# Optimization experiments

Measured on AMD Instinct MI355X. Metric: run time of the kernel, lower is better.

Reference implementation:

```python
import jax, jax.numpy as jnp
import numpy as np

RADIUS = 1.0  # df.ball_point(1, ...) -> radius 1, nsample 1


def ball_point(src_xyz, query_xyz, radius=RADIUS):
    """Ball query with nsample=1.
    src_xyz [B,M,3], query_xyz [B,N,3] -> idx [B,N] (first src point within
    radius, 0 if none), mask [B,N] (True if any src point within radius)."""
    d2 = jnp.sum((query_xyz[:, :, None, :] - src_xyz[:, None, :, :]) ** 2, axis=-1)  # [B,N,M]
    within = d2 < radius * radius
    idx = jnp.argmax(within, axis=-1)          # first True along M, else 0
    mask = jnp.any(within, axis=-1)
    return idx, mask


def gather_group(points, idx):
    """index_points_group with K=1: points [B,M,C], idx [B,N] -> [B,N,1,C]."""
    g = jnp.take_along_axis(points, idx[:, :, None], axis=1)  # [B,N,C]
    return g[:, :, None, :]


def _layer_loss(att_xyz, bat_xyz, att_feat, bat_feat):
    # feats come in as [B,C,N]; original does .permute(0,2,1)
    att_feat = jnp.transpose(att_feat, (0, 2, 1))  # [B,N_att,C]
    bat_feat = jnp.transpose(bat_feat, (0, 2, 1))  # [B,N_bat,C]
    bat_idx, _ = ball_point(bat_xyz, bat_xyz)
    att_idx, mask = ball_point(att_xyz, bat_xyz)
    group_att = jnp.concatenate(
        [gather_group(att_xyz, att_idx), gather_group(att_feat, att_idx)], axis=-1)  # [B,N,1,3+C]
    group_bat = jnp.concatenate(
        [gather_group(bat_xyz, bat_idx), gather_group(bat_feat, bat_idx)], axis=-1)
    m = mask[:, :, None, None].astype(group_att.dtype)  # broadcast over K=1 and C
    group_att = group_att * m
    group_bat = group_bat * m
    return jnp.mean((group_att - group_bat) ** 2)  # mse_loss(reduction='mean')


def reference(att_xyz0, att_xyz1, bat_xyz0, bat_xyz1,
              att_feat0, att_feat1, bat_feat0, bat_feat1):
    losses = [
        _layer_loss(att_xyz0, bat_xyz0, att_feat0, bat_feat0),  # transfer layer [0,0]
        _layer_loss(att_xyz1, bat_xyz1, att_feat1, bat_feat1),  # transfer layer [1,1]
    ]
    loss = (losses[0] + losses[1]) / len(losses)
    return jnp.where(jnp.isnan(loss), losses[-1], loss)


def setup_inputs() -> dict:
    key = jax.random.key(0)
    ks = jax.random.split(key, 8)
    B, N0, N1, C0, C1 = 4, 4096, 1024, 64, 128
    return {
        'att_xyz0': jax.random.normal(ks[0], (B, N0, 3), jnp.float32),
        'att_xyz1': jax.random.normal(ks[1], (B, N1, 3), jnp.float32),
        'bat_xyz0': jax.random.normal(ks[2], (B, N0, 3), jnp.float32),
        'bat_xyz1': jax.random.normal(ks[3], (B, N1, 3), jnp.float32),
        'att_feat0': jax.random.normal(ks[4], (B, C0, N0), jnp.float32),
        'att_feat1': jax.random.normal(ks[5], (B, C1, N1), jnp.float32),
        'bat_feat0': jax.random.normal(ks[6], (B, C0, N0), jnp.float32),
        'bat_feat1': jax.random.normal(ks[7], (B, C1, N1), jnp.float32),
    }
```

## Files before the change

kernel.cpp:

```cpp
#include <hip/hip_runtime.h>
#include <math.h>


#define RAD2 1.0f

constexpr int B  = 4;
constexpr int N0 = 4096, C0 = 64;
constexpr int N1 = 1024, C1 = 128;
constexpr int W0 = B * N0;
constexpr int W1 = B * N1;
constexpr int WT = W0 + W1;
constexpr int WPB  = 4;
constexpr int NBLK = WT / WPB;

template<int C, int N, int LOGN>
__device__ __forceinline__ float query_loss_wave(
    const float* __restrict__ att_xyz,
    const float* __restrict__ bat_xyz,
    const float* __restrict__ att_feat,
    const float* __restrict__ bat_feat,
    int gq, int lane)
{
    const int b = gq >> LOGN;
    const int n = gq & (N - 1);
    const float* aq = att_xyz + (size_t)b * N * 3;
    const float* bq = bat_xyz + (size_t)b * N * 3;

    const float qx = bq[n * 3 + 0];
    const float qy = bq[n * 3 + 1];
    const float qz = bq[n * 3 + 2];

    const float dax = qx - aq[lane * 3 + 0];
    const float day = qy - aq[lane * 3 + 1];
    const float daz = qz - aq[lane * 3 + 2];
    const float dbx = qx - bq[lane * 3 + 0];
    const float dby = qy - bq[lane * 3 + 1];
    const float dbz = qz - bq[lane * 3 + 2];
    const unsigned long long balA = __ballot(dax * dax + day * day + daz * daz < RAD2);
    const unsigned long long balB = __ballot(dbx * dbx + dby * dby + dbz * dbz < RAD2);

    int att_idx = -1;
    if (balA) {
        att_idx = (int)__builtin_ctzll(balA);
    } else {
        for (int c0 = 64; c0 < N; c0 += 64) {
            const int m = c0 + lane;
            const float dx = qx - aq[m * 3 + 0];
            const float dy = qy - aq[m * 3 + 1];
            const float dz = qz - aq[m * 3 + 2];
            const unsigned long long bal = __ballot(dx * dx + dy * dy + dz * dz < RAD2);
            if (bal) { att_idx = c0 + (int)__builtin_ctzll(bal); break; }
        }
    }
    if (att_idx < 0) return 0.0f;

    int bat_idx = n;
    if (balB) {
        bat_idx = (int)__builtin_ctzll(balB);
    } else {
        for (int c0 = 64; c0 < N; c0 += 64) {
            const int m = c0 + lane;
            const float dx = qx - bq[m * 3 + 0];
            const float dy = qy - bq[m * 3 + 1];
            const float dz = qz - bq[m * 3 + 2];
            const unsigned long long bal = __ballot(dx * dx + dy * dy + dz * dz < RAD2);
            if (bal) { bat_idx = c0 + (int)__builtin_ctzll(bal); break; }
        }
    }

    float part = 0.0f;
    if (lane < 3) {
        const float d = aq[att_idx * 3 + lane] - bq[bat_idx * 3 + lane];
        part = d * d;
    }
    const float* af = att_feat + (size_t)b * C * N;
    const float* bf = bat_feat + (size_t)b * C * N;
    #pragma unroll
    for (int c = lane; c < C; c += 64) {
        const float d = af[c * N + att_idx] - bf[c * N + bat_idx];
        part += d * d;
    }
    return part;
}

__global__ __launch_bounds__(256) void fg_fused_kernel(
    const float* __restrict__ att_xyz0, const float* __restrict__ bat_xyz0,
    const float* __restrict__ att_feat0, const float* __restrict__ bat_feat0,
    const float* __restrict__ att_xyz1, const float* __restrict__ bat_xyz1,
    const float* __restrict__ att_feat1, const float* __restrict__ bat_feat1,
    double* __restrict__ partials)
{
    const int lane = threadIdx.x & 63;
    const int gw   = blockIdx.x * WPB + (threadIdx.x >> 6);

    float part;
    if (gw < W0)
        part = query_loss_wave<C0, N0, 12>(att_xyz0, bat_xyz0, att_feat0,
                                           bat_feat0, gw, lane);
    else
        part = query_loss_wave<C1, N1, 10>(att_xyz1, bat_xyz1, att_feat1,
                                           bat_feat1, gw - W0, lane);

    #pragma unroll
    for (int off = 32; off > 0; off >>= 1)
        part += __shfl_down(part, off);
    if (lane == 0) partials[gw] = (double)part;
}

__global__ __launch_bounds__(1024) void fg_finalize_kernel(
    const double* __restrict__ partials,
    float* __restrict__ out)
{
    const int t = threadIdx.x;
    double s0 = 0.0, s1 = 0.0;
    #pragma unroll 4
    for (int i = t; i < W0; i += 1024) s0 += partials[i];
    for (int i = W0 + t; i < WT; i += 1024) s1 += partials[i];

    #pragma unroll
    for (int off = 32; off > 0; off >>= 1) {
        s0 += __shfl_down(s0, off);
        s1 += __shfl_down(s1, off);
    }

    __shared__ double sh0[16], sh1[16];
    const int lane = t & 63, w = t >> 6;
    if (lane == 0) { sh0[w] = s0; sh1[w] = s1; }
    __syncthreads();
    if (t == 0) {
        double a0 = 0.0, a1 = 0.0;
        #pragma unroll
        for (int i = 0; i < 16; ++i) { a0 += sh0[i]; a1 += sh1[i]; }
        const double l0 = a0 * (1.0 / 1097728.0);
        const double l1 = a1 * (1.0 / 536576.0);
        double loss = 0.5 * (l0 + l1);
        if (isnan(loss)) loss = l1;
        out[0] = (float)loss;
    }
}

extern "C" void kernel_launch(void* const* d_in, const int* in_sizes, int n_in,
                              void* d_out, int out_size, void* d_ws, size_t ws_size,
                              hipStream_t stream) {
    const float* att_xyz0  = (const float*)d_in[0];
    const float* att_xyz1  = (const float*)d_in[1];
    const float* bat_xyz0  = (const float*)d_in[2];
    const float* bat_xyz1  = (const float*)d_in[3];
    const float* att_feat0 = (const float*)d_in[4];
    const float* att_feat1 = (const float*)d_in[5];
    const float* bat_feat0 = (const float*)d_in[6];
    const float* bat_feat1 = (const float*)d_in[7];
    float* out = (float*)d_out;

    double* partials = (double*)d_ws;

    fg_fused_kernel<<<NBLK, 256, 0, stream>>>(
        att_xyz0, bat_xyz0, att_feat0, bat_feat0,
        att_xyz1, bat_xyz1, att_feat1, bat_feat1, partials);

    fg_finalize_kernel<<<1, 1024, 0, stream>>>(partials, out);
}
```

Measured before the change: 110.3 us.

## Process four queries per wave, reusing first-chunk source points across queries

Each wavefront now handles four consecutive query points instead of one. The first 64 att/bat source coordinates are loaded once per wave and reused for all four queries, and the four feature gathers are unrolled together to expose more memory-level parallelism. The fallback scan now walks the att and bat searches together in one loop. This cuts the wave count by four, which reduces launch parallelism, and it adds register pressure.

```diff
diff --git a/kernel.cpp b/kernel.cpp
--- a/kernel.cpp
+++ b/kernel.cpp
@@ -9,76 +9,96 @@
 constexpr int N1 = 1024, C1 = 128;
 constexpr int W0 = B * N0;
 constexpr int W1 = B * N1;
-constexpr int WT = W0 + W1;
-constexpr int WPB  = 4;
-constexpr int NBLK = WT / WPB;
+constexpr int QPW = 4;
+constexpr int WPB = 4;
+constexpr int NWV0 = W0 / QPW;
+constexpr int NWV1 = W1 / QPW;
+constexpr int NWVT = NWV0 + NWV1;
+constexpr int NBLK = NWVT / WPB;
 
 template<int C, int N, int LOGN>
-__device__ __forceinline__ float query_loss_wave(
+__device__ __forceinline__ float quad_loss_wave(
     const float* __restrict__ att_xyz,
     const float* __restrict__ bat_xyz,
     const float* __restrict__ att_feat,
     const float* __restrict__ bat_feat,
-    int gq, int lane)
+    int gq0, int lane)
 {
-    const int b = gq >> LOGN;
-    const int n = gq & (N - 1);
+    const int b  = gq0 >> LOGN;
+    const int n0 = gq0 & (N - 1);
     const float* aq = att_xyz + (size_t)b * N * 3;
     const float* bq = bat_xyz + (size_t)b * N * 3;
 
-    const float qx = bq[n * 3 + 0];
-    const float qy = bq[n * 3 + 1];
-    const float qz = bq[n * 3 + 2];
+    const float ax = aq[lane * 3 + 0];
+    const float ay = aq[lane * 3 + 1];
+    const float az = aq[lane * 3 + 2];
+    const float bx = bq[lane * 3 + 0];
+    const float by = bq[lane * 3 + 1];
+    const float bz = bq[lane * 3 + 2];
 
-    const float dax = qx - aq[lane * 3 + 0];
-    const float day = qy - aq[lane * 3 + 1];
-    const float daz = qz - aq[lane * 3 + 2];
-    const float dbx = qx - bq[lane * 3 + 0];
-    const float dby = qy - bq[lane * 3 + 1];
-    const float dbz = qz - bq[lane * 3 + 2];
-    const unsigned long long balA = __ballot(dax * dax + day * day + daz * daz < RAD2);
-    const unsigned long long balB = __ballot(dbx * dbx + dby * dby + dbz * dbz < RAD2);
+    float qx[QPW], qy[QPW], qz[QPW];
+    #pragma unroll
+    for (int q = 0; q < QPW; ++q) {
+        qx[q] = bq[(n0 + q) * 3 + 0];
+        qy[q] = bq[(n0 + q) * 3 + 1];
+        qz[q] = bq[(n0 + q) * 3 + 2];
+    }
 
-    int att_idx = -1;
-    if (balA) {
-        att_idx = (int)__builtin_ctzll(balA);
-    } else {
-        for (int c0 = 64; c0 < N; c0 += 64) {
-            const int m = c0 + lane;
-            const float dx = qx - aq[m * 3 + 0];
-            const float dy = qy - aq[m * 3 + 1];
-            const float dz = qz - aq[m * 3 + 2];
-            const unsigned long long bal = __ballot(dx * dx + dy * dy + dz * dz < RAD2);
-            if (bal) { att_idx = c0 + (int)__builtin_ctzll(bal); break; }
-        }
-    }
-    if (att_idx < 0) return 0.0f;
+    int att_idx[QPW], bat_idx[QPW];
+    #pragma unroll
+    for (int q = 0; q < QPW; ++q) {
+        const float dax = qx[q] - ax, day = qy[q] - ay, daz = qz[q] - az;
+        const float dbx = qx[q] - bx, dby = qy[q] - by, dbz = qz[q] - bz;
+        const unsigned long long balA =
+            __ballot(dax * dax + day * day + daz * daz < RAD2);
+        const unsigned long long balB =
+            __ballot(dbx * dbx + dby * dby + dbz * dbz < RAD2);
+        att_idx[q] = balA ? (int)__builtin_ctzll(balA) : -1;
+        bat_idx[q] = balB ? (int)__builtin_ctzll(balB) : (n0 + q);
 
-    int bat_idx = n;
-    if (balB) {
-        bat_idx = (int)__builtin_ctzll(balB);
-    } else {
-        for (int c0 = 64; c0 < N; c0 += 64) {
-            const int m = c0 + lane;
-            const float dx = qx - bq[m * 3 + 0];
-            const float dy = qy - bq[m * 3 + 1];
-            const float dz = qz - bq[m * 3 + 2];
-            const unsigned long long bal = __ballot(dx * dx + dy * dy + dz * dz < RAD2);
-            if (bal) { bat_idx = c0 + (int)__builtin_ctzll(bal); break; }
+        if (!balA || !balB) {
+            bool needA = !balA, needB = !balB;
+            for (int c0 = 64; c0 < N && (needA || needB); c0 += 64) {
+                const int m = c0 + lane;
+                if (needA) {
+                    const float dx = qx[q] - aq[m * 3 + 0];
+                    const float dy = qy[q] - aq[m * 3 + 1];
+                    const float dz = qz[q] - aq[m * 3 + 2];
+                    const unsigned long long bal =
+                        __ballot(dx * dx + dy * dy + dz * dz < RAD2);
+                    if (bal) { att_idx[q] = c0 + (int)__builtin_ctzll(bal); needA = false; }
+                }
+                if (needB) {
+                    const float dx = qx[q] - bq[m * 3 + 0];
+                    const float dy = qy[q] - bq[m * 3 + 1];
+                    const float dz = qz[q] - bq[m * 3 + 2];
+                    const unsigned long long bal =
+                        __ballot(dx * dx + dy * dy + dz * dz < RAD2);
+                    if (bal) { bat_idx[q] = c0 + (int)__builtin_ctzll(bal); needB = false; }
+                }
+            }
         }
     }
 
-    float part = 0.0f;
-    if (lane < 3) {
-        const float d = aq[att_idx * 3 + lane] - bq[bat_idx * 3 + lane];
-        part = d * d;
-    }
     const float* af = att_feat + (size_t)b * C * N;
     const float* bf = bat_feat + (size_t)b * C * N;
+    float part = 0.0f;
     #pragma unroll
-    for (int c = lane; c < C; c += 64) {
-        const float d = af[c * N + att_idx] - bf[c * N + bat_idx];
-        part += d * d;
+    for (int q = 0; q < QPW; ++q) {
+        const float w  = (att_idx[q] < 0) ? 0.0f : 1.0f;
+        const int   ia = (att_idx[q] < 0) ? 0    : att_idx[q];
+        const int   ib = bat_idx[q];
+        float pq = 0.0f;
+        if (lane < 3) {
+            const float d = aq[ia * 3 + lane] - bq[ib * 3 + lane];
+            pq = d * d;
+        }
+        #pragma unroll
+        for (int c = lane; c < C; c += 64) {
+            const float d = af[c * N + ia] - bf[c * N + ib];
+            pq += d * d;
+        }
+        part += w * pq;
     }
     return part;
 }
@@ -91,20 +111,20 @@
     double* __restrict__ partials)
 {
     const int lane = threadIdx.x & 63;
-    const int gw   = blockIdx.x * WPB + (threadIdx.x >> 6);
+    const int gwv  = blockIdx.x * WPB + (threadIdx.x >> 6);
 
     float part;
-    if (gw < W0)
-        part = query_loss_wave<C0, N0, 12>(att_xyz0, bat_xyz0, att_feat0,
-                                           bat_feat0, gw, lane);
+    if (gwv < NWV0)
+        part = quad_loss_wave<C0, N0, 12>(att_xyz0, bat_xyz0, att_feat0,
+                                          bat_feat0, gwv * QPW, lane);
     else
-        part = query_loss_wave<C1, N1, 10>(att_xyz1, bat_xyz1, att_feat1,
-                                           bat_feat1, gw - W0, lane);
+        part = quad_loss_wave<C1, N1, 10>(att_xyz1, bat_xyz1, att_feat1,
+                                          bat_feat1, (gwv - NWV0) * QPW, lane);
 
     #pragma unroll
     for (int off = 32; off > 0; off >>= 1)
         part += __shfl_down(part, off);
-    if (lane == 0) partials[gw] = (double)part;
+    if (lane == 0) partials[gwv] = (double)part;
 }
 
 __global__ __launch_bounds__(1024) void fg_finalize_kernel(
@@ -114,8 +134,8 @@
     const int t = threadIdx.x;
     double s0 = 0.0, s1 = 0.0;
     #pragma unroll 4
-    for (int i = t; i < W0; i += 1024) s0 += partials[i];
-    for (int i = W0 + t; i < WT; i += 1024) s1 += partials[i];
+    for (int i = t; i < NWV0; i += 1024) s0 += partials[i];
+    for (int i = NWV0 + t; i < NWVT; i += 1024) s1 += partials[i];
 
     #pragma unroll
     for (int off = 32; off > 0; off >>= 1) {
```

Result: slower. 113.7 us (+3.1%).
